# Optimization experiments

Measured on AMD Instinct MI355X. Metric: run time of the kernel, lower is better.

Reference implementation:

```python
import jax, jax.numpy as jnp
import numpy as np

LRELU_SLOPE = 0.2
ACT_GAIN = np.float32(np.sqrt(2.0))  # bias_act lrelu gain in StyleGAN2


def _per_sample_conv3x3(x, w):
    """Grouped-conv-as-batch trick: per-sample 3x3 conv.
    x: [B, C, H, W], w: [B, O, C, 3, 3] -> [B, O, H, W] (padding=1)."""
    def one(xi, wi):
        return jax.lax.conv_general_dilated(
            xi[None], wi, window_strides=(1, 1), padding=[(1, 1), (1, 1)],
            dimension_numbers=('NCHW', 'OIHW', 'NCHW'))[0]
    return jax.vmap(one)(x, w)


def setup_inputs() -> dict:
    key = jax.random.key(0)
    ks = jax.random.split(key, 10)
    B, C, R, W_DIM, IMG_C = 16, 512, 64, 512, 3
    inv_sqrt_c = np.float32(1.0 / np.sqrt(W_DIM))
    return {
        'ws': jax.random.normal(ks[0], (B, 2, W_DIM), jnp.float32),
        'const': jax.random.normal(ks[1], (C, R, R), jnp.float32),
        'conv_w': jax.random.normal(ks[2], (C, C, 3, 3), jnp.float32),
        'conv_b': jnp.zeros((C,), jnp.float32),
        'conv_aff_w': jax.random.normal(ks[3], (C, W_DIM), jnp.float32) * inv_sqrt_c,
        'conv_aff_b': jnp.ones((C,), jnp.float32),
        'noise_const': jax.random.normal(ks[4], (R, R), jnp.float32),
        'noise_strength': jnp.full((1,), 0.1, jnp.float32),
        'rgb_w': jax.random.normal(ks[5], (IMG_C, C, 1, 1), jnp.float32),
        'rgb_b': jnp.zeros((IMG_C,), jnp.float32),
        'rgb_aff_w': jax.random.normal(ks[6], (C, W_DIM), jnp.float32) * inv_sqrt_c,
        'rgb_aff_b': jnp.ones((C,), jnp.float32),
    }


def reference(ws, const, conv_w, conv_b, conv_aff_w, conv_aff_b,
              noise_const, noise_strength, rgb_w, rgb_b, rgb_aff_w, rgb_aff_b):
    B = ws.shape[0]
    # const input broadcast to batch (in_channels == 0 block)
    x = jnp.broadcast_to(const[None], (B,) + const.shape)

    # --- SynthesisLayer: modulated_conv2d (demodulate=True, fused_modconv=True) ---
    s = ws[:, 0] @ conv_aff_w.T + conv_aff_b                    # [B, C] styles
    w = conv_w[None] * s[:, None, :, None, None]                # [B, O, C, 3, 3] modulate
    dcoefs = jax.lax.rsqrt(jnp.sum(jnp.square(w), axis=(2, 3, 4)) + 1e-8)  # [B, O]
    w = w * dcoefs[:, :, None, None, None]                      # demodulate
    x = _per_sample_conv3x3(x, w)                               # grouped conv trick
    x = x + noise_const[None, None] * noise_strength            # fused noise add
    x = jax.nn.leaky_relu(x + conv_b[None, :, None, None], LRELU_SLOPE) * ACT_GAIN

    # --- ToRGBLayer: modulated 1x1 conv, demodulate=False ---
    weight_gain = np.float32(1.0 / np.sqrt(conv_w.shape[1]))    # 1/sqrt(in_ch*kh*kw)
    s2 = (ws[:, 1] @ rgb_aff_w.T + rgb_aff_b) * weight_gain     # [B, C]
    img = jnp.einsum('bchw,oc,bc->bohw', x, rgb_w[:, :, 0, 0], s2)
    img = img + rgb_b[None, :, None, None]
    return x, img
```

## Files before the change

### kernel.cpp

```cpp
#include <hip/hip_runtime.h>
#include <hip/hip_bf16.h>

typedef __attribute__((ext_vector_type(8))) short short8;
typedef __attribute__((ext_vector_type(4))) float f32x4;
typedef __attribute__((ext_vector_type(16))) float f32x16;

#define LRELU_SLOPE 0.2f
#define ACT_GAIN 1.41421356237309515f
#define WG_RGB 0.04419417382415922f

__device__ __forceinline__ void glds16(const short* g, short* l) {
    __builtin_amdgcn_global_load_lds(
        (const __attribute__((address_space(1))) unsigned int*)g,
        (__attribute__((address_space(3))) unsigned int*)l, 16, 0, 0);
}

__global__ void k_init(__hip_bfloat16* __restrict__ Ypad,
                       const float* __restrict__ rgb_b, float* __restrict__ img) {
    int blk = blockIdx.x, tid = threadIdx.x;
    if (blk < 1040) {
        int gslot = blk*4 + (tid >> 6);
        int b = gslot / 260;
        int cell = gslot - b*260;
        int h, w;
        if (cell < 66)       { h = 0;          w = cell; }
        else if (cell < 132) { h = 65;         w = cell - 66; }
        else if (cell < 196) { h = cell - 131; w = 0; }
        else                 { h = cell - 195; w = 65; }
        short8 z = {};
        *(short8*)((short*)Ypad + (((b*66 + h)*66) + w)*512 + (tid & 63)*8) = z;
    } else {
        int blk2 = blk - 1040;
        #pragma unroll
        for (int j = 0; j < 4; ++j) {
            int f4 = blk2*1024 + j*256 + tid;
            int b3 = f4 >> 10;
            int o3 = b3 % 3;
            float v = rgb_b[o3];
            f32x4 vv = {v, v, v, v};
            *(f32x4*)(img + f4*4) = vv;
        }
    }
}

__global__ void k_styles(const float* __restrict__ wsin,
                         const float* __restrict__ caw, const float* __restrict__ cab,
                         const float* __restrict__ raw_, const float* __restrict__ rab,
                         float* __restrict__ sbuf, float* __restrict__ s2buf) {
    int b = blockIdx.x, which = blockIdx.y;
    int tid = threadIdx.x, lane = tid & 63, wv = tid >> 6;
    const float* aw = which ? raw_ : caw;
    const float* ab = which ? rab : cab;
    float scale = which ? WG_RGB : 1.0f;
    float* op = which ? s2buf : sbuf;
    __shared__ float wsv[512];
    wsv[tid]       = wsin[(b*2 + which)*512 + tid];
    wsv[tid + 256] = wsin[(b*2 + which)*512 + tid + 256];
    __syncthreads();
    for (int c = wv; c < 512; c += 4) {
        float p = 0.f;
        #pragma unroll
        for (int kk = 0; kk < 8; ++kk)
            p += aw[c*512 + kk*64 + lane] * wsv[kk*64 + lane];
        #pragma unroll
        for (int off = 32; off; off >>= 1) p += __shfl_down(p, off, 64);
        if (lane == 0) op[b*512 + c] = (p + ab[c]) * scale;
    }
}

__global__ __launch_bounds__(256) void k_prepw(const float* __restrict__ conv_w,
                        float* __restrict__ w2sum, __hip_bfloat16* __restrict__ Abf) {
    int o = blockIdx.x, tid = threadIdx.x;
    __shared__ float wrow[4608];
    const f32x4* src = (const f32x4*)(conv_w + o*4608);
    #pragma unroll
    for (int r = 0; r < 5; ++r) {
        int idx = tid + (r << 8);
        if (idx < 1152) *(f32x4*)&wrow[idx*4] = src[idx];
    }
    __syncthreads();
    #pragma unroll
    for (int j = 0; j < 2; ++j) {
        int c = tid + (j << 8);
        float sum = 0.f;
        #pragma unroll
        for (int t = 0; t < 9; ++t) {
            float v = wrow[c*9 + t];
            sum += v*v;
            Abf[(t*512 + o)*512 + c] = __float2bfloat16(v);
        }
        w2sum[o*512 + c] = sum;
    }
}

__global__ __launch_bounds__(256) void k_dcoef(const float* __restrict__ sbuf,
                                               const float* __restrict__ w2sum,
                                               const float* __restrict__ s2buf,
                                               const float* __restrict__ rgb_w,
                                               float* __restrict__ dcoef,
                                               float* __restrict__ rgbc) {
    int gw = blockIdx.x*4 + (threadIdx.x >> 6);
    int lane = threadIdx.x & 63;
    int b = gw >> 9, o = gw & 511;
    float acc = 0.f;
    #pragma unroll
    for (int i = 0; i < 8; ++i) {
        int c = (i << 6) + lane;
        float sv = sbuf[(b << 9) + c];
        acc += sv*sv*w2sum[(o << 9) + c];
    }
    #pragma unroll
    for (int off = 32; off; off >>= 1) acc += __shfl_down(acc, off, 64);
    if (lane == 0) dcoef[(b << 9) + o] = rsqrtf(acc + 1e-8f);
    if (blockIdx.x < 96) {
        int flat = blockIdx.x*256 + threadIdx.x;
        int bb = flat / 1536;
        int r  = flat - bb*1536;
        int c  = r & 511;
        rgbc[flat] = rgb_w[r] * s2buf[bb*512 + c];
    }
}

__global__ void k_ypad(const float* __restrict__ cst, const float* __restrict__ sbuf,
                       __hip_bfloat16* __restrict__ Ypad) {
    int b = blockIdx.x >> 6, h = blockIdx.x & 63, tid = threadIdx.x;
    __shared__ float tile[64][65];
    for (int cc = 0; cc < 8; ++cc) {
        int c0 = cc << 6;
        #pragma unroll
        for (int it = 0; it < 16; ++it) {
            int cl = (it << 2) + (tid >> 6);
            int w = tid & 63;
            tile[cl][w] = cst[(c0 + cl)*4096 + (h << 6) + w];
        }
        __syncthreads();
        #pragma unroll
        for (int it = 0; it < 16; ++it) {
            int flat = (it << 8) + tid;
            int w = flat >> 6, cl = flat & 63;
            float v = sbuf[(b << 9) + c0 + cl] * tile[cl][w];
            Ypad[(((b*66 + h + 1)*66) + (w + 1))*512 + c0 + cl] = __float2bfloat16(v);
        }
        __syncthreads();
    }
}

__global__ __launch_bounds__(512, 2) void conv_gemm(
    const short* __restrict__ Abf,
    const short* __restrict__ Ypad,
    const float* __restrict__ dcoef,
    const float* __restrict__ noise,
    const float* __restrict__ nstr,
    const float* __restrict__ bias,
    const float* __restrict__ rgbc,
    float* __restrict__ xout,
    float* __restrict__ img)
{
    __shared__ short Aring[32768];
    __shared__ short Bh2[25344];
    __shared__ float red[256][3][2];

    int tid = threadIdx.x, lane = tid & 63, wv = tid >> 6;
    int wr = wv >> 2, wc = wv & 3;
    int ml32 = lane & 31, hi = lane >> 5;

    int blk = blockIdx.x;
    int xcd = blk & 7, idx = blk >> 3;
    int v = xcd * 64 + idx;
    int mblk = v & 1, nblk = v >> 1;
    int b = nblk >> 4;
    int hw0 = (nblk & 15) << 8;
    int h0 = hw0 >> 6;
    int o0 = mblk << 8;

    int bgofs[3];
    #pragma unroll
    for (int r = 0; r < 3; ++r) {
        int i = tid + (r << 9);
        int pos = i >> 2;
        int hl = pos / 66;
        int ww = pos - hl*66;
        int q  = (i & 3) ^ ((pos >> 1) & 3);
        bgofs[r] = (((b*66 + h0 + hl)*66) + ww)*512 + q*8;
    }
    int pos4 = 384 + (lane >> 2);
    int q4 = (lane & 3) ^ ((pos4 >> 1) & 3);
    int bg4 = ((b*66 + h0 + 5)*66 + (pos4 - 330))*512 + q4*8;

    int agofs[2];
    #pragma unroll
    for (int r = 0; r < 2; ++r) {
        int s = tid + (r << 9);
        int row = s >> 2;
        int q = (s & 3) ^ ((row >> 1) & 3);
        agofs[r] = ((o0 + row) << 9) + q*8;
    }

    int aro[4], arx[4];
    #pragma unroll
    for (int mi = 0; mi < 4; ++mi) {
        int row = wr*128 + mi*32 + ml32;
        aro[mi] = row*32;
        arx[mi] = (row >> 1) & 3;
    }
    int pb0 = wc*66 + ml32;
    const int BPA[9] = {0, 1, 2, 66, 67, 68, 132, 133, 134};

    short* AW = Aring + wv*512;

    f32x16 acc[4][2] = {};
    short8 fa0[4], fb0[2], fa1[4], fb1[2];

    #pragma unroll
    for (int r = 0; r < 3; ++r)
        glds16(Ypad + bgofs[r], Bh2 + wv*512 + r*4096);
    if (lane < 48) glds16(Ypad + bg4, Bh2 + 12288);
    #pragma unroll
    for (int t = 0; t < 3; ++t) {
        glds16(Abf + (t << 18) + agofs[0], AW + t*8192);
        glds16(Abf + (t << 18) + agofs[1], AW + t*8192 + 4096);
    }
    asm volatile("s_waitcnt vmcnt(2)" ::: "memory");
    __builtin_amdgcn_s_barrier();
    {
        int pos_ = pb0;
        int x_ = (pos_ >> 1) & 3;
        #pragma unroll
        for (int mi = 0; mi < 4; ++mi)
            fa0[mi] = *(const short8*)(Aring + aro[mi] + ((hi ^ arx[mi]) << 3));
        #pragma unroll
        for (int ni = 0; ni < 2; ++ni)
            fb0[ni] = *(const short8*)(Bh2 + (pos_ + ni*32)*32 + ((hi ^ x_) << 3));
    }

    const int VMP[9] = {3, 4, 4, 4, 3, 2, 2, 2, 2};

#define MMCL(FA, FB)                                                            \
    __builtin_amdgcn_s_setprio(1);                                              \
    _Pragma("unroll")                                                           \
    for (int mi = 0; mi < 4; ++mi)                                              \
        _Pragma("unroll")                                                       \
        for (int ni = 0; ni < 2; ++ni)                                          \
            acc[mi][ni] = __builtin_amdgcn_mfma_f32_32x32x16_bf16(              \
                FA[mi], FB[ni], acc[mi][ni], 0, 0, 0);                          \
    __builtin_amdgcn_s_setprio(0);

#define PHASE(TAP, HC, C0, C0N, RB)                                             \
    {                                                                           \
        int rr  = ((RB) + (TAP)) & 3;                                           \
        int rrN = ((RB) + (TAP) + 1) & 3;                                       \
        int rw  = ((RB) + (TAP) + 3) & 3;                                       \
        constexpr int TAPN = ((TAP) + 1) % 9;                                   \
        constexpr int TAPP = ((TAP) < 6) ? (TAP) + 3 : (TAP) - 6;               \
        constexpr int HN = (HC) ^ 1;                                            \
        constexpr int HRA = ((TAP) == 8) ? HN : (HC);                           \
                                  \
        { int pos_ = pb0 + BPA[(TAP)]; int x_ = (pos_ >> 1) & 3;                \
          _Pragma("unroll")                                                     \
          for (int mi = 0; mi < 4; ++mi)                                        \
              fa1[mi] = *(const short8*)(Aring + rr*8192 + aro[mi]              \
                                         + (((2 + hi) ^ arx[mi]) << 3));        \
          _Pragma("unroll")                                                     \
          for (int ni = 0; ni < 2; ++ni)                                        \
              fb1[ni] = *(const short8*)(Bh2 + (HC)*12672 + (pos_ + ni*32)*32   \
                                         + (((2 + hi) ^ x_) << 3));             \
        }                                                                       \
                         \
        { const short* asrc_ = Abf + (TAPP << 18) + (((TAP) < 6) ? (C0) : (C0N)); \
          glds16(asrc_ + agofs[0], AW + rw*8192);                               \
          glds16(asrc_ + agofs[1], AW + rw*8192 + 4096); }                      \
        if ((TAP) < 3)                                                          \
            glds16(Ypad + bgofs[(TAP)] + (C0N),                                 \
                   Bh2 + HN*12672 + wv*512 + (TAP)*4096);                       \
        if ((TAP) == 3) {                                                       \
            if (lane < 48) glds16(Ypad + bg4 + (C0N), Bh2 + HN*12672 + 12288);  \
        }                                                                       \
        __builtin_amdgcn_sched_barrier(0);                                      \
        MMCL(fa0, fb0)                                                          \
        __builtin_amdgcn_sched_barrier(0);                                      \
                                \
        { int pos_ = pb0 + BPA[TAPN]; int x_ = (pos_ >> 1) & 3;                 \
          _Pragma("unroll")                                                     \
          for (int mi = 0; mi < 4; ++mi)                                        \
              fa0[mi] = *(const short8*)(Aring + rrN*8192 + aro[mi]             \
                                         + ((hi ^ arx[mi]) << 3));              \
          _Pragma("unroll")                                                     \
          for (int ni = 0; ni < 2; ++ni)                                        \
              fb0[ni] = *(const short8*)(Bh2 + HRA*12672 + (pos_ + ni*32)*32    \
                                         + ((hi ^ x_) << 3));                   \
        }                                                                       \
        __builtin_amdgcn_sched_barrier(0);                                      \
        MMCL(fa1, fb1)                                                          \
        asm volatile("s_waitcnt vmcnt(%0)" :: "i"(VMP[(TAP)]) : "memory");      \
        __builtin_amdgcn_s_barrier();                                           \
    }

#define CHUNK9(HC, C0, C0N, RB)                                                 \
    PHASE(0, HC, C0, C0N, RB) PHASE(1, HC, C0, C0N, RB)                         \
    PHASE(2, HC, C0, C0N, RB) PHASE(3, HC, C0, C0N, RB)                         \
    PHASE(4, HC, C0, C0N, RB) PHASE(5, HC, C0, C0N, RB)                         \
    PHASE(6, HC, C0, C0N, RB) PHASE(7, HC, C0, C0N, RB)                         \
    PHASE(8, HC, C0, C0N, RB)

    for (int cc = 0; cc < 8; ++cc) {
        int c0e = cc << 6;
        int rbe = (cc << 1) & 3;
        CHUNK9(0, c0e, c0e + 32, rbe)
        int c0o = c0e + 32;
        int c0no = (c0e + 64) & 511;
        int rbo = (rbe + 1) & 3;
        CHUNK9(1, c0o, c0no, rbo)
    }
#undef PHASE
#undef CHUNK9
#undef MMCL

    float ns = nstr[0];
    float pr0[2] = {0.f, 0.f}, pr1[2] = {0.f, 0.f}, pr2[2] = {0.f, 0.f};
    #pragma unroll
    for (int mi = 0; mi < 4; ++mi) {
        int ob = o0 + wr*128 + mi*32 + hi*4;
        f32x4 dc[4], bs[4], c0r[4], c1r[4], c2r[4];
        #pragma unroll
        for (int g = 0; g < 4; ++g) {
            dc[g]  = *(const f32x4*)(dcoef + (b << 9) + ob + g*8);
            bs[g]  = *(const f32x4*)(bias + ob + g*8);
            c0r[g] = *(const f32x4*)(rgbc + b*1536 + ob + g*8);
            c1r[g] = *(const f32x4*)(rgbc + b*1536 + 512 + ob + g*8);
            c2r[g] = *(const f32x4*)(rgbc + b*1536 + 1024 + ob + g*8);
        }
        #pragma unroll
        for (int ni = 0; ni < 2; ++ni) {
            int nl = wc*64 + ni*32 + ml32;
            int hw = hw0 + nl;
            float nz = noise[hw] * ns;
            #pragma unroll
            for (int g = 0; g < 4; ++g)
                #pragma unroll
                for (int t = 0; t < 4; ++t) {
                    float vv = acc[mi][ni][g*4 + t] * dc[g][t] + nz + bs[g][t];
                    vv = (vv < 0.f ? LRELU_SLOPE*vv : vv) * ACT_GAIN;
                    xout[(((b << 9) + ob + g*8 + t) << 12) + hw] = vv;
                    pr0[ni] += vv * c0r[g][t];
                    pr1[ni] += vv * c1r[g][t];
                    pr2[ni] += vv * c2r[g][t];
                }
        }
    }
    #pragma unroll
    for (int ni = 0; ni < 2; ++ni) {
        pr0[ni] += __shfl_down(pr0[ni], 32, 64);
        pr1[ni] += __shfl_down(pr1[ni], 32, 64);
        pr2[ni] += __shfl_down(pr2[ni], 32, 64);
    }
    if (lane < 32) {
        #pragma unroll
        for (int ni = 0; ni < 2; ++ni) {
            int nl = wc*64 + ni*32 + ml32;
            red[nl][0][wr] = pr0[ni];
            red[nl][1][wr] = pr1[ni];
            red[nl][2][wr] = pr2[ni];
        }
    }
    __syncthreads();
    for (int p = tid; p < 768; p += 512) {
        int o3 = p >> 8, nl = p & 255;
        atomicAdd(img + ((b*3 + o3) << 12) + hw0 + nl, red[nl][o3][0] + red[nl][o3][1]);
    }
}

extern "C" void kernel_launch(void* const* d_in, const int* in_sizes, int n_in,
                              void* d_out, int out_size, void* d_ws, size_t ws_size,
                              hipStream_t stream) {
    (void)in_sizes; (void)n_in; (void)out_size; (void)ws_size;
    const float* wsin   = (const float*)d_in[0];
    const float* cst    = (const float*)d_in[1];
    const float* conv_w = (const float*)d_in[2];
    const float* conv_b = (const float*)d_in[3];
    const float* caw    = (const float*)d_in[4];
    const float* cab    = (const float*)d_in[5];
    const float* noise  = (const float*)d_in[6];
    const float* nstr   = (const float*)d_in[7];
    const float* rgb_w  = (const float*)d_in[8];
    const float* rgb_b  = (const float*)d_in[9];
    const float* raw_   = (const float*)d_in[10];
    const float* rab    = (const float*)d_in[11];

    char* wsb = (char*)d_ws;
    float* sbuf   = (float*)(wsb + 0);
    float* s2buf  = (float*)(wsb + 32768);
    float* dcoef  = (float*)(wsb + 65536);
    float* rgbc   = (float*)(wsb + 98304);
    float* w2sum  = (float*)(wsb + 196608);
    __hip_bfloat16* Abf  = (__hip_bfloat16*)(wsb + 1245184);
    __hip_bfloat16* Ypad = (__hip_bfloat16*)(wsb + 5963776);

    float* xout = (float*)d_out;
    float* img  = xout + 33554432;

    k_init<<<1088, 256, 0, stream>>>(Ypad, rgb_b, img);
    k_styles<<<dim3(16, 2), 256, 0, stream>>>(wsin, caw, cab, raw_, rab, sbuf, s2buf);
    k_prepw<<<512, 256, 0, stream>>>(conv_w, w2sum, Abf);
    k_dcoef<<<2048, 256, 0, stream>>>(sbuf, w2sum, s2buf, rgb_w, dcoef, rgbc);
    k_ypad<<<1024, 256, 0, stream>>>(cst, sbuf, Ypad);
    conv_gemm<<<512, 512, 0, stream>>>((const short*)Abf, (const short*)Ypad,
                                       dcoef, noise, nstr, conv_b, rgbc, xout, img);
}
```

Baseline: 574.3 us.

## Shrink conv GEMM tile to 256x128 with 16-channel K chunks and 256 threads

Restructures the implicit-GEMM conv kernel from 512-thread blocks covering 256 outputs by 256 pixels to 256-thread blocks covering 256 outputs by 128 pixels, doubling the grid to 1024 blocks. The K chunk per tap shrinks from 32 to 16 channels, with a new XOR swizzle, a single B halo buffer reloaded at tap 0, and double-buffered fragment registers. Shared memory is cut sharply and the reduction buffer now aliases it, which should allow more resident blocks per CU and better load balance. In exchange it adds more barriers per unit of MFMA work, reloads more halo data per output, and exposes the B-tile load at tap 0 where it was previously prefetched.

```diff
diff --git a/kernel.cpp b/kernel.cpp
--- a/kernel.cpp
+++ b/kernel.cpp
@@ -145,7 +145,7 @@
     }
 }
 
-__global__ __launch_bounds__(512, 2) void conv_gemm(
+__global__ __launch_bounds__(256, 2) void conv_gemm(
     const short* __restrict__ Abf,
     const short* __restrict__ Ypad,
     const float* __restrict__ dcoef,
@@ -156,164 +156,133 @@
     float* __restrict__ xout,
     float* __restrict__ img)
 {
-    __shared__ short Aring[32768];
-    __shared__ short Bh2[25344];
-    __shared__ float red[256][3][2];
+    __shared__ short SH[22528];
+    short* Aring = SH;
+    short* Bbuf  = SH + 16384;
+    float (*red)[3][2] = (float (*)[3][2])SH;
 
     int tid = threadIdx.x, lane = tid & 63, wv = tid >> 6;
-    int wr = wv >> 2, wc = wv & 3;
+    int wr = wv >> 1, wc = wv & 1;
     int ml32 = lane & 31, hi = lane >> 5;
 
     int blk = blockIdx.x;
     int xcd = blk & 7, idx = blk >> 3;
-    int v = xcd * 64 + idx;
+    int v = xcd * 128 + idx;
     int mblk = v & 1, nblk = v >> 1;
-    int b = nblk >> 4;
-    int hw0 = (nblk & 15) << 8;
-    int h0 = hw0 >> 6;
+    int b = nblk >> 5;
+    int n0 = (nblk & 31) << 7;
+    int h0 = n0 >> 6;
     int o0 = mblk << 8;
 
     int bgofs[3];
     #pragma unroll
     for (int r = 0; r < 3; ++r) {
-        int i = tid + (r << 9);
-        int pos = i >> 2;
-        int hl = pos / 66;
-        int ww = pos - hl*66;
-        int q  = (i & 3) ^ ((pos >> 1) & 3);
+        int s = tid + (r << 8);
+        int pos = s >> 1; if (pos > 263) pos = 263;
+        int q = (s & 1) ^ (((pos >> 2) ^ (pos >> 3)) & 1);
+        int hl = pos / 66, ww = pos - hl * 66;
         bgofs[r] = (((b*66 + h0 + hl)*66) + ww)*512 + q*8;
     }
-    int pos4 = 384 + (lane >> 2);
-    int q4 = (lane & 3) ^ ((pos4 >> 1) & 3);
-    int bg4 = ((b*66 + h0 + 5)*66 + (pos4 - 330))*512 + q4*8;
-
     int agofs[2];
     #pragma unroll
     for (int r = 0; r < 2; ++r) {
-        int s = tid + (r << 9);
-        int row = s >> 2;
-        int q = (s & 3) ^ ((row >> 1) & 3);
+        int s = tid + (r << 8);
+        int row = s >> 1;
+        int q = (s & 1) ^ (((row >> 2) ^ (row >> 3)) & 1);
         agofs[r] = ((o0 + row) << 9) + q*8;
     }
-
-    int aro[4], arx[4];
+    int aro[4];
     #pragma unroll
     for (int mi = 0; mi < 4; ++mi) {
         int row = wr*128 + mi*32 + ml32;
-        aro[mi] = row*32;
-        arx[mi] = (row >> 1) & 3;
+        aro[mi] = row*16 + ((hi ^ (((row >> 2) ^ (row >> 3)) & 1)) << 3);
     }
     int pb0 = wc*66 + ml32;
-    const int BPA[9] = {0, 1, 2, 66, 67, 68, 132, 133, 134};
 
     short* AW = Aring + wv*512;
+    short* BW = Bbuf + wv*512;
 
     f32x16 acc[4][2] = {};
-    short8 fa0[4], fb0[2], fa1[4], fb1[2];
-
-    #pragma unroll
-    for (int r = 0; r < 3; ++r)
-        glds16(Ypad + bgofs[r], Bh2 + wv*512 + r*4096);
-    if (lane < 48) glds16(Ypad + bg4, Bh2 + 12288);
+    short8 fa[2][4], fb[2][2];
+
     #pragma unroll
     for (int t = 0; t < 3; ++t) {
-        glds16(Abf + (t << 18) + agofs[0], AW + t*8192);
-        glds16(Abf + (t << 18) + agofs[1], AW + t*8192 + 4096);
-    }
-    asm volatile("s_waitcnt vmcnt(2)" ::: "memory");
+        glds16(Abf + (t << 18) + agofs[0], AW + t*4096);
+        glds16(Abf + (t << 18) + agofs[1], AW + t*4096 + 2048);
+    }
+    asm volatile("s_waitcnt vmcnt(0)" ::: "memory");
     __builtin_amdgcn_s_barrier();
-    {
-        int pos_ = pb0;
-        int x_ = (pos_ >> 1) & 3;
-        #pragma unroll
-        for (int mi = 0; mi < 4; ++mi)
-            fa0[mi] = *(const short8*)(Aring + aro[mi] + ((hi ^ arx[mi]) << 3));
-        #pragma unroll
-        for (int ni = 0; ni < 2; ++ni)
-            fb0[ni] = *(const short8*)(Bh2 + (pos_ + ni*32)*32 + ((hi ^ x_) << 3));
-    }
-
-    const int VMP[9] = {3, 4, 4, 4, 3, 2, 2, 2, 2};
-
-#define MMCL(FA, FB)                                                            \
-    __builtin_amdgcn_s_setprio(1);                                              \
-    _Pragma("unroll")                                                           \
-    for (int mi = 0; mi < 4; ++mi)                                              \
-        _Pragma("unroll")                                                       \
-        for (int ni = 0; ni < 2; ++ni)                                          \
-            acc[mi][ni] = __builtin_amdgcn_mfma_f32_32x32x16_bf16(              \
-                FA[mi], FB[ni], acc[mi][ni], 0, 0, 0);                          \
+
+#define FRAGRD(SET, SLOT, TAPX)                                             \
+    { _Pragma("unroll")                                                     \
+      for (int mi = 0; mi < 4; ++mi)                                        \
+          fa[SET][mi] = *(const short8*)(Aring + (SLOT)*4096 + aro[mi]);    \
+      _Pragma("unroll")                                                     \
+      for (int ni = 0; ni < 2; ++ni) {                                      \
+          int p_ = pb0 + ((TAPX)/3)*66 + ((TAPX)%3) + ni*32;                \
+          int jx = (hi ^ (((p_ >> 2) ^ (p_ >> 3)) & 1)) << 3;               \
+          fb[SET][ni] = *(const short8*)(Bbuf + p_*16 + jx); } }
+
+#define MMCL(SET)                                                           \
+    __builtin_amdgcn_s_setprio(1);                                          \
+    _Pragma("unroll")                                                       \
+    for (int mi = 0; mi < 4; ++mi)                                          \
+        _Pragma("unroll")                                                   \
+        for (int ni = 0; ni < 2; ++ni)                                      \
+            acc[mi][ni] = __builtin_amdgcn_mfma_f32_32x32x16_bf16(          \
+                fa[SET][mi], fb[SET][ni], acc[mi][ni], 0, 0, 0);            \
     __builtin_amdgcn_s_setprio(0);
 
-#define PHASE(TAP, HC, C0, C0N, RB)                                             \
-    {                                                                           \
-        int rr  = ((RB) + (TAP)) & 3;                                           \
-        int rrN = ((RB) + (TAP) + 1) & 3;                                       \
-        int rw  = ((RB) + (TAP) + 3) & 3;                                       \
-        constexpr int TAPN = ((TAP) + 1) % 9;                                   \
-        constexpr int TAPP = ((TAP) < 6) ? (TAP) + 3 : (TAP) - 6;               \
-        constexpr int HN = (HC) ^ 1;                                            \
-        constexpr int HRA = ((TAP) == 8) ? HN : (HC);                           \
-                                  \
-        { int pos_ = pb0 + BPA[(TAP)]; int x_ = (pos_ >> 1) & 3;                \
-          _Pragma("unroll")                                                     \
-          for (int mi = 0; mi < 4; ++mi)                                        \
-              fa1[mi] = *(const short8*)(Aring + rr*8192 + aro[mi]              \
-                                         + (((2 + hi) ^ arx[mi]) << 3));        \
-          _Pragma("unroll")                                                     \
-          for (int ni = 0; ni < 2; ++ni)                                        \
-              fb1[ni] = *(const short8*)(Bh2 + (HC)*12672 + (pos_ + ni*32)*32   \
-                                         + (((2 + hi) ^ x_) << 3));             \
-        }                                                                       \
-                         \
+#define PHASE(TAP, CUR, C0, C0N, RB)                                        \
+    {                                                                       \
+        int rr  = ((RB) + (TAP)) & 3;                                       \
+        int rrN = ((RB) + (TAP) + 1) & 3;                                   \
+        int rw  = ((RB) + (TAP) + 3) & 3;                                   \
+        constexpr int TAPN = ((TAP) + 1) % 9;                               \
+        constexpr int TAPP = ((TAP) < 6) ? (TAP) + 3 : (TAP) - 6;           \
+        constexpr int NXT = (CUR) ^ 1;                                      \
+        if ((TAP) == 0) {                                                   \
+            glds16(Ypad + bgofs[0] + (C0), BW);                             \
+            glds16(Ypad + bgofs[1] + (C0), BW + 2048);                      \
+            glds16(Ypad + bgofs[2] + (C0), BW + 4096);                      \
+        }                                                                   \
         { const short* asrc_ = Abf + (TAPP << 18) + (((TAP) < 6) ? (C0) : (C0N)); \
-          glds16(asrc_ + agofs[0], AW + rw*8192);                               \
-          glds16(asrc_ + agofs[1], AW + rw*8192 + 4096); }                      \
-        if ((TAP) < 3)                                                          \
-            glds16(Ypad + bgofs[(TAP)] + (C0N),                                 \
-                   Bh2 + HN*12672 + wv*512 + (TAP)*4096);                       \
-        if ((TAP) == 3) {                                                       \
-            if (lane < 48) glds16(Ypad + bg4 + (C0N), Bh2 + HN*12672 + 12288);  \
-        }                                                                       \
-        __builtin_amdgcn_sched_barrier(0);                                      \
-        MMCL(fa0, fb0)                                                          \
-        __builtin_amdgcn_sched_barrier(0);                                      \
-                                \
-        { int pos_ = pb0 + BPA[TAPN]; int x_ = (pos_ >> 1) & 3;                 \
-          _Pragma("unroll")                                                     \
-          for (int mi = 0; mi < 4; ++mi)                                        \
-              fa0[mi] = *(const short8*)(Aring + rrN*8192 + aro[mi]             \
-                                         + ((hi ^ arx[mi]) << 3));              \
-          _Pragma("unroll")                                                     \
-          for (int ni = 0; ni < 2; ++ni)                                        \
-              fb0[ni] = *(const short8*)(Bh2 + HRA*12672 + (pos_ + ni*32)*32    \
-                                         + ((hi ^ x_) << 3));                   \
-        }                                                                       \
-        __builtin_amdgcn_sched_barrier(0);                                      \
-        MMCL(fa1, fb1)                                                          \
-        asm volatile("s_waitcnt vmcnt(%0)" :: "i"(VMP[(TAP)]) : "memory");      \
-        __builtin_amdgcn_s_barrier();                                           \
-    }
-
-#define CHUNK9(HC, C0, C0N, RB)                                                 \
-    PHASE(0, HC, C0, C0N, RB) PHASE(1, HC, C0, C0N, RB)                         \
-    PHASE(2, HC, C0, C0N, RB) PHASE(3, HC, C0, C0N, RB)                         \
-    PHASE(4, HC, C0, C0N, RB) PHASE(5, HC, C0, C0N, RB)                         \
-    PHASE(6, HC, C0, C0N, RB) PHASE(7, HC, C0, C0N, RB)                         \
-    PHASE(8, HC, C0, C0N, RB)
-
-    for (int cc = 0; cc < 8; ++cc) {
-        int c0e = cc << 6;
+          glds16(asrc_ + agofs[0], AW + rw*4096);                           \
+          glds16(asrc_ + agofs[1], AW + rw*4096 + 2048); }                  \
+        if ((TAP) == 0) {                                                   \
+            asm volatile("s_waitcnt vmcnt(2)" ::: "memory");                \
+            __builtin_amdgcn_s_barrier();                                   \
+            FRAGRD(CUR, rr, 0)                                              \
+        }                                                                   \
+        if ((TAP) < 8) { FRAGRD(NXT, rrN, TAPN) }                           \
+        __builtin_amdgcn_sched_barrier(0);                                  \
+        MMCL(CUR)                                                           \
+        asm volatile("s_waitcnt vmcnt(2)" ::: "memory");                    \
+        __builtin_amdgcn_s_barrier();                                       \
+    }
+
+#define CHUNK9(PAR, C0, C0N, RB)                                            \
+    PHASE(0, ((0+(PAR))&1), C0, C0N, RB) PHASE(1, ((1+(PAR))&1), C0, C0N, RB) \
+    PHASE(2, ((2+(PAR))&1), C0, C0N, RB) PHASE(3, ((3+(PAR))&1), C0, C0N, RB) \
+    PHASE(4, ((4+(PAR))&1), C0, C0N, RB) PHASE(5, ((5+(PAR))&1), C0, C0N, RB) \
+    PHASE(6, ((6+(PAR))&1), C0, C0N, RB) PHASE(7, ((7+(PAR))&1), C0, C0N, RB) \
+    PHASE(8, ((8+(PAR))&1), C0, C0N, RB)
+
+    for (int cc = 0; cc < 16; ++cc) {
+        int c0e = cc << 5;
         int rbe = (cc << 1) & 3;
-        CHUNK9(0, c0e, c0e + 32, rbe)
-        int c0o = c0e + 32;
-        int c0no = (c0e + 64) & 511;
-        int rbo = (rbe + 1) & 3;
-        CHUNK9(1, c0o, c0no, rbo)
+        CHUNK9(0, c0e, c0e + 16, rbe)
+        int c0o = c0e + 16;
+        int c0no = (c0e + 32) & 511;
+        CHUNK9(1, c0o, c0no, (rbe + 1) & 3)
     }
 #undef PHASE
 #undef CHUNK9
+#undef FRAGRD
 #undef MMCL
+
+    asm volatile("s_waitcnt vmcnt(0)" ::: "memory");
+    __builtin_amdgcn_s_barrier();
 
     float ns = nstr[0];
     float pr0[2] = {0.f, 0.f}, pr1[2] = {0.f, 0.f}, pr2[2] = {0.f, 0.f};
@@ -332,7 +301,7 @@
         #pragma unroll
         for (int ni = 0; ni < 2; ++ni) {
             int nl = wc*64 + ni*32 + ml32;
-            int hw = hw0 + nl;
+            int hw = n0 + nl;
             float nz = noise[hw] * ns;
             #pragma unroll
             for (int g = 0; g < 4; ++g)
@@ -363,9 +332,9 @@
         }
     }
     __syncthreads();
-    for (int p = tid; p < 768; p += 512) {
-        int o3 = p >> 8, nl = p & 255;
-        atomicAdd(img + ((b*3 + o3) << 12) + hw0 + nl, red[nl][o3][0] + red[nl][o3][1]);
+    for (int p = tid; p < 384; p += 256) {
+        int o3 = p >> 7, nl = p & 127;
+        atomicAdd(img + ((b*3 + o3) << 12) + n0 + nl, red[nl][o3][0] + red[nl][o3][1]);
     }
 }
 
@@ -403,6 +372,6 @@
     k_prepw<<<512, 256, 0, stream>>>(conv_w, w2sum, Abf);
     k_dcoef<<<2048, 256, 0, stream>>>(sbuf, w2sum, s2buf, rgb_w, dcoef, rgbc);
     k_ypad<<<1024, 256, 0, stream>>>(cst, sbuf, Ypad);
-    conv_gemm<<<512, 512, 0, stream>>>((const short*)Abf, (const short*)Ypad,
-                                       dcoef, noise, nstr, conv_b, rgbc, xout, img);
-}
+    conv_gemm<<<1024, 256, 0, stream>>>((const short*)Abf, (const short*)Ypad,
+                                        dcoef, noise, nstr, conv_b, rgbc, xout, img);
+}
```

Measured after the change: 667.7 us. 1.16x slower.
